# Kernel tuning notes

Hardware: AMD Instinct MI355X
Metric: run time of the kernel (lower is better)

Reference implementation:

```python
import jax, jax.numpy as jnp
import numpy as np

B, T, D_MODEL, H, D = 2, 2048, 2048, 16, 128


def _rope_tables(t, d_half, base=10000.0):
    inv_freq = 1.0 / (base ** (jnp.arange(d_half, dtype=jnp.float32) / d_half))
    ang = jnp.arange(t, dtype=jnp.float32)[:, None] * inv_freq[None, :]  # (T, D/2)
    return jnp.cos(ang), jnp.sin(ang)


def setup_inputs() -> dict:
    key = jax.random.key(0)
    ks = jax.random.split(key, 5)
    x = jax.random.normal(ks[0], (B, T, D_MODEL), dtype=jnp.float32)
    mask = jnp.tril(jnp.ones((T, T), dtype=bool))  # causal boolean mask
    cos, sin = _rope_tables(T, D // 2)
    std = 1.0 / np.sqrt(D_MODEL)
    Wq = jax.random.normal(ks[1], (D_MODEL, H * D), dtype=jnp.float32) * std
    Wk = jax.random.normal(ks[2], (D_MODEL, H * D), dtype=jnp.float32) * std
    Wv = jax.random.normal(ks[3], (D_MODEL, H * D), dtype=jnp.float32) * std
    Wo = jax.random.normal(ks[4], (H * D, D_MODEL), dtype=jnp.float32) * std
    return {"x": x, "mask": mask, "cos": cos, "sin": sin,
            "Wq": Wq, "Wk": Wk, "Wv": Wv, "Wo": Wo}


def _apply_rope(x, cos, sin):
    # x: (B, H, T, D); cos/sin: (T, D/2)
    half = x.shape[-1] // 2
    x1, x2 = x[..., :half], x[..., half:]
    c = cos[None, None]
    s = sin[None, None]
    return jnp.concatenate([x1 * c - x2 * s, x1 * s + x2 * c], axis=-1)


def reference(x, mask, cos, sin, Wq, Wk, Wv, Wo):
    b, t, _ = x.shape
    scale = 1.0 / np.sqrt(D)
    # projections: (B, T, H*D) -> (B, H, T, D)
    q = (x @ Wq).reshape(b, t, H, D).transpose(0, 2, 1, 3)
    k = (x @ Wk).reshape(b, t, H, D).transpose(0, 2, 1, 3)
    v = (x @ Wv).reshape(b, t, H, D).transpose(0, 2, 1, 3)
    q = _apply_rope(q, cos, sin)
    k = _apply_rope(k, cos, sin)
    scores = jnp.einsum('bhqd,bhkd->bhqk', q, k) * scale
    scores = jnp.where(mask[None, None], scores, jnp.float32(-1e30))
    attn = jax.nn.softmax(scores, axis=-1)
    out = jnp.einsum('bhqk,bhkd->bhqd', attn, v)  # (B, H, T, D)
    out = out.transpose(0, 2, 1, 3).reshape(b, t, H * D)
    return out @ Wo
```

## Files before the change

### kernel.cpp

```cpp
#include <hip/hip_runtime.h>

#define T_SEQ 2048
#define DM    2048
#define NH    16
#define HD    128
#define NROW  4096

typedef __attribute__((ext_vector_type(8))) short short8;
typedef __attribute__((ext_vector_type(4))) float f32x4;
typedef __attribute__((ext_vector_type(16))) float f32x16;

static __device__ __forceinline__ float bf2f(unsigned short h) {
    unsigned int u = ((unsigned int)h) << 16;
    return __builtin_bit_cast(float, u);
}
static __device__ __forceinline__ unsigned short f2bf(float f) {
    unsigned int u = __builtin_bit_cast(unsigned int, f);
    u += 0x7FFFu + ((u >> 16) & 1u);
    return (unsigned short)(u >> 16);
}
static __device__ __forceinline__ unsigned short bf_fast(float f) {
    return (unsigned short)((__builtin_bit_cast(unsigned int, f) + 0x8000u) >> 16);
}

typedef __attribute__((address_space(1))) const unsigned int gas_uint;
typedef __attribute__((address_space(3))) unsigned int las_uint;

static __device__ __forceinline__ void load_lds16(const void* g, void* l) {
    __builtin_amdgcn_global_load_lds((gas_uint*)g, (las_uint*)l, 16, 0, 0);
}

static __device__ __forceinline__ f32x4 mfma_bf16(short8 a, short8 b, f32x4 c) {
    return __builtin_amdgcn_mfma_f32_16x16x32_bf16(a, b, c, 0, 0, 0);
}
static __device__ __forceinline__ f32x16 mfma32_bf16(short8 a, short8 b, f32x16 c) {
    return __builtin_amdgcn_mfma_f32_32x32x16_bf16(a, b, c, 0, 0, 0);
}

__global__ __launch_bounds__(256) void k_prep(const float* __restrict__ x,
                                              unsigned short* __restrict__ xb,
                                              const float* __restrict__ w0, const float* __restrict__ w1,
                                              const float* __restrict__ w2, const float* __restrict__ w3,
                                              unsigned short* __restrict__ t0, unsigned short* __restrict__ t1,
                                              unsigned short* __restrict__ t2, unsigned short* __restrict__ t3) {
    const int tid = threadIdx.x;
    const int z = blockIdx.z;
    if (z == 4) {
        const int iblock = blockIdx.y * 32 + blockIdx.x;
#pragma unroll
        for (int i = 0; i < 8; ++i) {
            int idx = (iblock * 2048 + i * 256 + tid) * 4;
            float4 v = *(const float4*)(x + idx);
            ushort4 o;
            o.x = f2bf(v.x); o.y = f2bf(v.y); o.z = f2bf(v.z); o.w = f2bf(v.w);
            *(ushort4*)(xb + idx) = o;
        }
        return;
    }
    __shared__ unsigned short tile[64][68];
    const float* W = (z == 0) ? w0 : (z == 1) ? w1 : (z == 2) ? w2 : w3;
    unsigned short* Wt = (z == 0) ? t0 : (z == 1) ? t1 : (z == 2) ? t2 : t3;
    const int bx = blockIdx.x * 64;
    const int by = blockIdx.y * 64;
    const int rr = tid >> 4, cc = (tid & 15) * 4;
#pragma unroll
    for (int it = 0; it < 4; ++it) {
        int row = it * 16 + rr;
        float4 v = *(const float4*)(W + (size_t)(by + row) * DM + bx + cc);
        ushort4 o;
        o.x = f2bf(v.x); o.y = f2bf(v.y); o.z = f2bf(v.z); o.w = f2bf(v.w);
        *(ushort4*)&tile[row][cc] = o;
    }
    __syncthreads();
#pragma unroll
    for (int it = 0; it < 4; ++it) {
        int ln = it * 16 + rr;
        ushort4 v;
#pragma unroll
        for (int j = 0; j < 4; ++j) v = (j == 0) ? (ushort4){tile[cc][ln], 0, 0, 0} : v, ((unsigned short*)&v)[j] = tile[cc + j][ln];
        *(ushort4*)(Wt + (size_t)(bx + ln) * DM + by + cc) = v;
    }
}

template <bool FOUT>
static __device__ __forceinline__ void gemm_body(const unsigned short* __restrict__ A,
                                                 const unsigned short* __restrict__ Bt,
                                                 unsigned short* __restrict__ Cb,
                                                 float* __restrict__ Cf) {
    __shared__ unsigned short As[128 * 64];
    __shared__ unsigned short Bs[128 * 64];
    const int tid = threadIdx.x;
    const int w = tid >> 6, lane = tid & 63;
    const int col = lane & 15, quad = lane >> 4;
    const int wm = w >> 1, wn = w & 1;
    const size_t m0 = (size_t)blockIdx.y * 128;
    const size_t n0 = (size_t)blockIdx.x * 128;

    f32x4 acc[4][4];
#pragma unroll
    for (int i = 0; i < 4; ++i)
#pragma unroll
        for (int j = 0; j < 4; ++j)
            acc[i][j] = (f32x4){0.f, 0.f, 0.f, 0.f};

    const int lrow = lane >> 3;
    const int gcol = ((lane & 7) ^ lrow) * 8;

    for (int k0 = 0; k0 < DM; k0 += 64) {
#pragma unroll
        for (int c = w; c < 16; c += 4) {
            load_lds16(A + (m0 + c * 8 + lrow) * DM + k0 + gcol, &As[c * 512]);
            load_lds16(Bt + (n0 + c * 8 + lrow) * DM + k0 + gcol, &Bs[c * 512]);
        }
        __syncthreads();
#pragma unroll
        for (int ks = 0; ks < 2; ++ks) {
            short8 af[4], bf[4];
            int g = ks * 4 + quad;
#pragma unroll
            for (int mt = 0; mt < 4; ++mt) {
                int r = wm * 64 + mt * 16 + col;
                af[mt] = *(const short8*)&As[r * 64 + ((g ^ (r & 7)) * 8)];
            }
#pragma unroll
            for (int nt = 0; nt < 4; ++nt) {
                int r = wn * 64 + nt * 16 + col;
                bf[nt] = *(const short8*)&Bs[r * 64 + ((g ^ (r & 7)) * 8)];
            }
#pragma unroll
            for (int mt = 0; mt < 4; ++mt)
#pragma unroll
                for (int nt = 0; nt < 4; ++nt)
                    acc[mt][nt] = mfma_bf16(af[mt], bf[nt], acc[mt][nt]);
        }
        __syncthreads();
    }
#pragma unroll
    for (int mt = 0; mt < 4; ++mt)
#pragma unroll
        for (int nt = 0; nt < 4; ++nt)
#pragma unroll
            for (int reg = 0; reg < 4; ++reg) {
                size_t r = m0 + wm * 64 + mt * 16 + quad * 4 + reg;
                size_t c = n0 + wn * 64 + nt * 16 + col;
                if (FOUT) Cf[r * DM + c] = acc[mt][nt][reg];
                else      Cb[r * DM + c] = f2bf(acc[mt][nt][reg]);
            }
}

__global__ __launch_bounds__(256) void k_gemm_qkv(const unsigned short* __restrict__ xb,
                                                  const unsigned short* __restrict__ wtq,
                                                  const unsigned short* __restrict__ wtk,
                                                  const unsigned short* __restrict__ wtv,
                                                  unsigned short* __restrict__ qb,
                                                  unsigned short* __restrict__ kb,
                                                  unsigned short* __restrict__ vb) {
    int z = blockIdx.z;
    const unsigned short* Bt = (z == 0) ? wtq : (z == 1) ? wtk : wtv;
    unsigned short* C = (z == 0) ? qb : (z == 1) ? kb : vb;
    gemm_body<false>(xb, Bt, C, nullptr);
}

__global__ __launch_bounds__(256) void k_gemm_out(const unsigned short* __restrict__ ob,
                                                  const unsigned short* __restrict__ wto,
                                                  float* __restrict__ out) {
    gemm_body<true>(ob, wto, nullptr, out);
}

__global__ __launch_bounds__(256) void k_rope_k(unsigned short* __restrict__ K,
                                                const float* __restrict__ cosp,
                                                const float* __restrict__ sinp) {
    int idx = blockIdx.x * 256 + threadIdx.x;
    int d4 = (idx & 15) * 4;
    int h = (idx >> 4) & 15;
    int row = idx >> 8;
    int t = row & (T_SEQ - 1);
    size_t base = (size_t)row * DM + h * HD + d4;
    ushort4 x1 = *(const ushort4*)(K + base);
    ushort4 x2 = *(const ushort4*)(K + base + 64);
    float4 c = *(const float4*)(cosp + t * 64 + d4);
    float4 s = *(const float4*)(sinp + t * 64 + d4);
    ushort4 o1, o2;
#pragma unroll
    for (int i = 0; i < 4; ++i) {
        float a1 = bf2f(((const unsigned short*)&x1)[i]);
        float a2 = bf2f(((const unsigned short*)&x2)[i]);
        float cc = ((const float*)&c)[i], ss = ((const float*)&s)[i];
        ((unsigned short*)&o1)[i] = f2bf(a1 * cc - a2 * ss);
        ((unsigned short*)&o2)[i] = f2bf(a1 * ss + a2 * cc);
    }
    *(ushort4*)(K + base) = o1;
    *(ushort4*)(K + base + 64) = o2;
}

__global__ __launch_bounds__(256) void k_vtr(const unsigned short* __restrict__ V,
                                             unsigned short* __restrict__ Vt) {
    __shared__ unsigned short tile[64][68];
    int t0 = blockIdx.x * 64;
    int hd0 = blockIdx.y * 64;
    int b = blockIdx.z;
    int tid = threadIdx.x;
    int rr = tid >> 4, cc = (tid & 15) * 4;
#pragma unroll
    for (int it = 0; it < 4; ++it) {
        int row = it * 16 + rr;
        *(ushort4*)&tile[row][cc] =
            *(const ushort4*)(V + (size_t)(b * T_SEQ + t0 + row) * DM + hd0 + cc);
    }
    __syncthreads();
    int h = hd0 >> 7, d0 = hd0 & 127;
    size_t obase = (size_t)(b * NH + h) * HD;
#pragma unroll
    for (int it = 0; it < 4; ++it) {
        int lhd = it * 16 + rr;
        ushort4 v;
#pragma unroll
        for (int j = 0; j < 4; ++j) ((unsigned short*)&v)[j] = tile[cc + j][lhd];
        *(ushort4*)(Vt + (obase + d0 + lhd) * (size_t)T_SEQ + t0 + cc) = v;
    }
}

#define PST 72
__global__ __launch_bounds__(256) void k_flash(const unsigned short* __restrict__ Q,
                                               const unsigned short* __restrict__ K,
                                               const unsigned short* __restrict__ Vt,
                                               unsigned short* __restrict__ O,
                                               const float* __restrict__ cosp,
                                               const float* __restrict__ sinp) {
    __shared__ unsigned short Ks[64 * 128];
    __shared__ unsigned short Vs[128 * 64];
    __shared__ unsigned short Ps[4][32 * PST];
    const int tid = threadIdx.x;
    const int w = tid >> 6, lane = tid & 63;
    const int col = lane & 31, l5 = lane >> 5;
    const int flat = blockIdx.x | (blockIdx.y << 4) | (blockIdx.z << 8);
    const int j = 15 - (flat >> 5);
    const int hb = flat & 31;
    const int h = hb & 15, b = hb >> 4;
    const int q0 = j * 128;
    const size_t rowbase = ((size_t)b * T_SEQ) * DM + (size_t)h * HD;
    const size_t hbase = ((size_t)b * NH + h) * HD;
    const float SCL = 0.088388347648318447f * 1.4426950408889634f;
    unsigned short* Pw = &Ps[w][0];

    const int t = q0 + w * 32 + col;
    short8 qf[8];
    {
        const unsigned short* qp = Q + rowbase + (size_t)t * DM + l5 * 8;
#pragma unroll
        for (int st = 0; st < 8; ++st)
            qf[st] = *(const short8*)(qp + st * 16);
        const float* cp = cosp + t * 64 + l5 * 8;
        const float* sp = sinp + t * 64 + l5 * 8;
#pragma unroll
        for (int st = 0; st < 4; ++st) {
            float4 c0 = *(const float4*)(cp + st * 16);
            float4 c1 = *(const float4*)(cp + st * 16 + 4);
            float4 s0v = *(const float4*)(sp + st * 16);
            float4 s1v = *(const float4*)(sp + st * 16 + 4);
#pragma unroll
            for (int jj = 0; jj < 8; ++jj) {
                float cv = ((jj < 4) ? ((const float*)&c0)[jj] : ((const float*)&c1)[jj - 4]) * SCL;
                float sv = ((jj < 4) ? ((const float*)&s0v)[jj] : ((const float*)&s1v)[jj - 4]) * SCL;
                float a1 = bf2f((unsigned short)qf[st][jj]);
                float a2 = bf2f((unsigned short)qf[st + 4][jj]);
                qf[st][jj]     = (short)f2bf(a1 * cv - a2 * sv);
                qf[st + 4][jj] = (short)f2bf(a1 * sv + a2 * cv);
            }
        }
    }

    f32x16 o[4];
#pragma unroll
    for (int i = 0; i < 4; ++i) o[i] = (f32x16)(0.f);
    float m_i = -1e30f, l_i = 0.f;

    const int kt_max = 2 * j + 1;
    const int kt_lim = (q0 + w * 32 + 31) >> 6;
    const int cswz = col & 7;

    for (int kt = 0; kt <= kt_max; ++kt) {
        const int k0 = kt * 64;
        __syncthreads();
#pragma unroll
        for (int c = 0; c < 4; ++c) {
            const int c4 = w * 4 + c;
            const int krow = c4 * 4 + (lane >> 4);
            const int kpos = lane & 15;
            load_lds16(K + rowbase + (size_t)(k0 + krow) * DM + ((kpos ^ (krow & 7)) * 8),
                       &Ks[c4 * 512]);
            const int vrow = c4 * 8 + (lane >> 3);
            const int vpos = lane & 7;
            load_lds16(Vt + (hbase + vrow) * (size_t)T_SEQ + k0 + ((vpos ^ (vrow & 7)) * 8),
                       &Vs[c4 * 512]);
        }
        __syncthreads();
        if (kt > kt_lim) continue;

        f32x16 s0 = (f32x16)(0.f), s1 = (f32x16)(0.f);
        __builtin_amdgcn_s_setprio(1);
#pragma unroll
        for (int st = 0; st < 8; ++st) {
            const int dg = (2 * st + l5) ^ cswz;
            short8 kf0 = *(const short8*)&Ks[col * 128 + dg * 8];
            short8 kf1 = *(const short8*)&Ks[col * 128 + 4096 + dg * 8];
            s0 = mfma32_bf16(kf0, qf[st], s0);
            s1 = mfma32_bf16(kf1, qf[st], s1);
        }
        __builtin_amdgcn_s_setprio(0);

        if (k0 + 63 > q0 + w * 32) {
            const int kb = k0 + 4 * l5;
#pragma unroll
            for (int r = 0; r < 16; ++r) {
                const int key = kb + (r & 3) + 8 * (r >> 2);
                if (key > t) s0[r] = -1e30f;
                if (key + 32 > t) s1[r] = -1e30f;
            }
        }

        float mx = -1e30f;
#pragma unroll
        for (int r = 0; r < 16; ++r) mx = fmaxf(mx, fmaxf(s0[r], s1[r]));
        mx = fmaxf(mx, __shfl_xor(mx, 32));
        if (!__all(mx - m_i <= 8.0f)) {
            const float mnew = fmaxf(m_i, mx);
            const float alpha = __builtin_amdgcn_exp2f(m_i - mnew);
            m_i = mnew;
            l_i *= alpha;
#pragma unroll
            for (int i = 0; i < 4; ++i) o[i] *= alpha;
        }
        float sum = 0.f;
#pragma unroll
        for (int r = 0; r < 16; ++r) {
            float p0 = __builtin_amdgcn_exp2f(s0[r] - m_i);
            float p1 = __builtin_amdgcn_exp2f(s1[r] - m_i);
            s0[r] = p0; s1[r] = p1;
            sum += p0 + p1;
        }
        sum += __shfl_xor(sum, 32);
        l_i += sum;

#pragma unroll
        for (int g = 0; g < 4; ++g) {
            ushort4 a4, b4;
#pragma unroll
            for (int i = 0; i < 4; ++i) {
                ((unsigned short*)&a4)[i] = bf_fast(s0[g * 4 + i]);
                ((unsigned short*)&b4)[i] = bf_fast(s1[g * 4 + i]);
            }
            *(ushort4*)(Pw + col * PST + g * 8 + 4 * l5)      = a4;
            *(ushort4*)(Pw + col * PST + 32 + g * 8 + 4 * l5) = b4;
        }
        short8 pb[4];
#pragma unroll
        for (int st = 0; st < 4; ++st)
            pb[st] = *(const short8*)(Pw + col * PST + st * 16 + l5 * 8);

        __builtin_amdgcn_s_setprio(1);
#pragma unroll
        for (int ms = 0; ms < 4; ++ms) {
            const int drow = (ms * 32 + col) * 64;
#pragma unroll
            for (int st = 0; st < 4; ++st) {
                const int kg = (2 * st + l5) ^ cswz;
                short8 vf = *(const short8*)&Vs[drow + kg * 8];
                o[ms] = mfma32_bf16(vf, pb[st], o[ms]);
            }
        }
        __builtin_amdgcn_s_setprio(0);
    }

    const float inv = __builtin_amdgcn_rcpf(l_i);
    unsigned short* op = O + rowbase + (size_t)t * DM;
#pragma unroll
    for (int ms = 0; ms < 4; ++ms)
#pragma unroll
        for (int g = 0; g < 4; ++g) {
            ushort4 st4;
#pragma unroll
            for (int i = 0; i < 4; ++i)
                ((unsigned short*)&st4)[i] = bf_fast(o[ms][g * 4 + i] * inv);
            *(ushort4*)(op + ms * 32 + g * 8 + 4 * l5) = st4;
        }
}

extern "C" void kernel_launch(void* const* d_in, const int* in_sizes, int n_in,
                              void* d_out, int out_size, void* d_ws, size_t ws_size,
                              hipStream_t stream) {
    const float* x    = (const float*)d_in[0];
    const float* cosp = (const float*)d_in[2];
    const float* sinp = (const float*)d_in[3];
    const float* Wq   = (const float*)d_in[4];
    const float* Wk   = (const float*)d_in[5];
    const float* Wv   = (const float*)d_in[6];
    const float* Wo   = (const float*)d_in[7];
    float* out = (float*)d_out;

    unsigned short* xb  = (unsigned short*)d_ws;
    unsigned short* wtq = xb  + (size_t)NROW * DM;
    unsigned short* wtk = wtq + (size_t)DM * DM;
    unsigned short* wtv = wtk + (size_t)DM * DM;
    unsigned short* wto = wtv + (size_t)DM * DM;
    unsigned short* qb  = wto + (size_t)DM * DM;
    unsigned short* kb  = qb  + (size_t)NROW * DM;
    unsigned short* vb  = kb  + (size_t)NROW * DM;
    unsigned short* ob  = vb  + (size_t)NROW * DM;
    unsigned short* vt  = xb;

    hipLaunchKernelGGL(k_prep, dim3(32, 32, 5), dim3(256), 0, stream,
                       x, xb, Wq, Wk, Wv, Wo, wtq, wtk, wtv, wto);
    hipLaunchKernelGGL(k_gemm_qkv, dim3(16, 32, 3), dim3(256), 0, stream,
                       xb, wtq, wtk, wtv, qb, kb, vb);
    hipLaunchKernelGGL(k_rope_k, dim3(4096), dim3(256), 0, stream, kb, cosp, sinp);
    hipLaunchKernelGGL(k_vtr, dim3(32, 32, 2), dim3(256), 0, stream, vb, vt);
    hipLaunchKernelGGL(k_flash, dim3(16, 16, 2), dim3(256), 0, stream,
                       qb, kb, vt, ob, cosp, sinp);
    hipLaunchKernelGGL(k_gemm_out, dim3(16, 32, 1), dim3(256), 0, stream, ob, wto, out);
}
```

Measured before the change: 396.5 us.

## Fuse K RoPE and V transpose into QKV GEMM epilogues

The QKV projection GEMM now has per-slice epilogues. The K slice stages its tile in shared memory and applies RoPE before writing. The V slice writes directly in the transposed (b,h,d,t) layout the flash kernel expects. This removes the separate k_rope_k and k_vtr launches and their extra global read/write passes over K and V. In exchange, the QKV kernel uses more shared memory (about 33 KB), which may reduce occupancy, and the transposed V stores are 4-element strided writes that are less coalesced.

```diff
diff --git a/kernel.cpp b/kernel.cpp
--- a/kernel.cpp
+++ b/kernel.cpp
@@ -82,13 +82,16 @@
     }
 }
 
-template <bool FOUT>
-static __device__ __forceinline__ void gemm_body(const unsigned short* __restrict__ A,
+template <int MODE>
+static __device__ __forceinline__ void gemm_body(unsigned short* smem,
+                                                 const unsigned short* __restrict__ A,
                                                  const unsigned short* __restrict__ Bt,
                                                  unsigned short* __restrict__ Cb,
-                                                 float* __restrict__ Cf) {
-    __shared__ unsigned short As[128 * 64];
-    __shared__ unsigned short Bs[128 * 64];
+                                                 float* __restrict__ Cf,
+                                                 const float* __restrict__ cosp,
+                                                 const float* __restrict__ sinp) {
+    unsigned short* As = smem;
+    unsigned short* Bs = smem + 8192;
     const int tid = threadIdx.x;
     const int w = tid >> 6, lane = tid & 63;
     const int col = lane & 15, quad = lane >> 4;
@@ -135,17 +138,70 @@
         }
         __syncthreads();
     }
-#pragma unroll
-    for (int mt = 0; mt < 4; ++mt)
-#pragma unroll
-        for (int nt = 0; nt < 4; ++nt)
-#pragma unroll
-            for (int reg = 0; reg < 4; ++reg) {
-                size_t r = m0 + wm * 64 + mt * 16 + quad * 4 + reg;
-                size_t c = n0 + wn * 64 + nt * 16 + col;
-                if (FOUT) Cf[r * DM + c] = acc[mt][nt][reg];
-                else      Cb[r * DM + c] = f2bf(acc[mt][nt][reg]);
-            }
+
+    if (MODE == 0 || MODE == 1) {
+#pragma unroll
+        for (int mt = 0; mt < 4; ++mt)
+#pragma unroll
+            for (int nt = 0; nt < 4; ++nt)
+#pragma unroll
+                for (int reg = 0; reg < 4; ++reg) {
+                    size_t r = m0 + wm * 64 + mt * 16 + quad * 4 + reg;
+                    size_t c = n0 + wn * 64 + nt * 16 + col;
+                    if (MODE == 1) Cf[r * DM + c] = acc[mt][nt][reg];
+                    else           Cb[r * DM + c] = f2bf(acc[mt][nt][reg]);
+                }
+    } else if (MODE == 2) {
+        const int bb = (int)(m0 >> 11);
+        const int tb = ((int)m0 & 2047) + wm * 64 + quad * 4;
+#pragma unroll
+        for (int mt = 0; mt < 4; ++mt)
+#pragma unroll
+            for (int nt = 0; nt < 4; ++nt) {
+                const int c = (int)n0 + wn * 64 + nt * 16 + col;
+                ushort4 v;
+#pragma unroll
+                for (int reg = 0; reg < 4; ++reg)
+                    ((unsigned short*)&v)[reg] = f2bf(acc[mt][nt][reg]);
+                *(ushort4*)(Cb + (size_t)(bb * 2048 + c) * T_SEQ + tb + mt * 16) = v;
+            }
+    } else {
+        unsigned short* tile = smem;
+#pragma unroll
+        for (int mt = 0; mt < 4; ++mt)
+#pragma unroll
+            for (int nt = 0; nt < 4; ++nt)
+#pragma unroll
+                for (int reg = 0; reg < 4; ++reg) {
+                    const int rl = wm * 64 + mt * 16 + quad * 4 + reg;
+                    const int cl = wn * 64 + nt * 16 + col;
+                    tile[rl * 132 + cl] = f2bf(acc[mt][nt][reg]);
+                }
+        __syncthreads();
+#pragma unroll
+        for (int i = 0; i < 8; ++i) {
+            const int task = i * 256 + tid;
+            const int rl = task >> 4;
+            const int d4 = (task & 15) * 4;
+            const int r = (int)m0 + rl;
+            const int t = r & (T_SEQ - 1);
+            ushort4 x1 = *(const ushort4*)&tile[rl * 132 + d4];
+            ushort4 x2 = *(const ushort4*)&tile[rl * 132 + d4 + 64];
+            float4 c = *(const float4*)(cosp + t * 64 + d4);
+            float4 s = *(const float4*)(sinp + t * 64 + d4);
+            ushort4 o1, o2;
+#pragma unroll
+            for (int q = 0; q < 4; ++q) {
+                float a1 = bf2f(((const unsigned short*)&x1)[q]);
+                float a2 = bf2f(((const unsigned short*)&x2)[q]);
+                float cc = ((const float*)&c)[q], ss = ((const float*)&s)[q];
+                ((unsigned short*)&o1)[q] = f2bf(a1 * cc - a2 * ss);
+                ((unsigned short*)&o2)[q] = f2bf(a1 * ss + a2 * cc);
+            }
+            *(ushort4*)(Cb + (size_t)r * DM + n0 + d4)      = o1;
+            *(ushort4*)(Cb + (size_t)r * DM + n0 + d4 + 64) = o2;
+        }
+    }
 }
 
 __global__ __launch_bounds__(256) void k_gemm_qkv(const unsigned short* __restrict__ xb,
@@ -154,70 +210,21 @@
                                                   const unsigned short* __restrict__ wtv,
                                                   unsigned short* __restrict__ qb,
                                                   unsigned short* __restrict__ kb,
-                                                  unsigned short* __restrict__ vb) {
-    int z = blockIdx.z;
-    const unsigned short* Bt = (z == 0) ? wtq : (z == 1) ? wtk : wtv;
-    unsigned short* C = (z == 0) ? qb : (z == 1) ? kb : vb;
-    gemm_body<false>(xb, Bt, C, nullptr);
+                                                  unsigned short* __restrict__ vt,
+                                                  const float* __restrict__ cosp,
+                                                  const float* __restrict__ sinp) {
+    __shared__ unsigned short smem[16896];
+    const int z = blockIdx.z;
+    if (z == 0)      gemm_body<0>(smem, xb, wtq, qb, nullptr, nullptr, nullptr);
+    else if (z == 1) gemm_body<3>(smem, xb, wtk, kb, nullptr, cosp, sinp);
+    else             gemm_body<2>(smem, xb, wtv, vt, nullptr, nullptr, nullptr);
 }
 
 __global__ __launch_bounds__(256) void k_gemm_out(const unsigned short* __restrict__ ob,
                                                   const unsigned short* __restrict__ wto,
                                                   float* __restrict__ out) {
-    gemm_body<true>(ob, wto, nullptr, out);
-}
-
-__global__ __launch_bounds__(256) void k_rope_k(unsigned short* __restrict__ K,
-                                                const float* __restrict__ cosp,
-                                                const float* __restrict__ sinp) {
-    int idx = blockIdx.x * 256 + threadIdx.x;
-    int d4 = (idx & 15) * 4;
-    int h = (idx >> 4) & 15;
-    int row = idx >> 8;
-    int t = row & (T_SEQ - 1);
-    size_t base = (size_t)row * DM + h * HD + d4;
-    ushort4 x1 = *(const ushort4*)(K + base);
-    ushort4 x2 = *(const ushort4*)(K + base + 64);
-    float4 c = *(const float4*)(cosp + t * 64 + d4);
-    float4 s = *(const float4*)(sinp + t * 64 + d4);
-    ushort4 o1, o2;
-#pragma unroll
-    for (int i = 0; i < 4; ++i) {
-        float a1 = bf2f(((const unsigned short*)&x1)[i]);
-        float a2 = bf2f(((const unsigned short*)&x2)[i]);
-        float cc = ((const float*)&c)[i], ss = ((const float*)&s)[i];
-        ((unsigned short*)&o1)[i] = f2bf(a1 * cc - a2 * ss);
-        ((unsigned short*)&o2)[i] = f2bf(a1 * ss + a2 * cc);
-    }
-    *(ushort4*)(K + base) = o1;
-    *(ushort4*)(K + base + 64) = o2;
-}
-
-__global__ __launch_bounds__(256) void k_vtr(const unsigned short* __restrict__ V,
-                                             unsigned short* __restrict__ Vt) {
-    __shared__ unsigned short tile[64][68];
-    int t0 = blockIdx.x * 64;
-    int hd0 = blockIdx.y * 64;
-    int b = blockIdx.z;
-    int tid = threadIdx.x;
-    int rr = tid >> 4, cc = (tid & 15) * 4;
-#pragma unroll
-    for (int it = 0; it < 4; ++it) {
-        int row = it * 16 + rr;
-        *(ushort4*)&tile[row][cc] =
-            *(const ushort4*)(V + (size_t)(b * T_SEQ + t0 + row) * DM + hd0 + cc);
-    }
-    __syncthreads();
-    int h = hd0 >> 7, d0 = hd0 & 127;
-    size_t obase = (size_t)(b * NH + h) * HD;
-#pragma unroll
-    for (int it = 0; it < 4; ++it) {
-        int lhd = it * 16 + rr;
-        ushort4 v;
-#pragma unroll
-        for (int j = 0; j < 4; ++j) ((unsigned short*)&v)[j] = tile[cc + j][lhd];
-        *(ushort4*)(Vt + (obase + d0 + lhd) * (size_t)T_SEQ + t0 + cc) = v;
-    }
+    __shared__ unsigned short smem[16384];
+    gemm_body<1>(smem, ob, wto, nullptr, out, nullptr, nullptr);
 }
 
 #define PST 72
@@ -405,16 +412,13 @@
     unsigned short* wto = wtv + (size_t)DM * DM;
     unsigned short* qb  = wto + (size_t)DM * DM;
     unsigned short* kb  = qb  + (size_t)NROW * DM;
-    unsigned short* vb  = kb  + (size_t)NROW * DM;
-    unsigned short* ob  = vb  + (size_t)NROW * DM;
-    unsigned short* vt  = xb;
+    unsigned short* vt  = kb  + (size_t)NROW * DM;
+    unsigned short* ob  = vt  + (size_t)NROW * DM;
 
     hipLaunchKernelGGL(k_prep, dim3(32, 32, 5), dim3(256), 0, stream,
                        x, xb, Wq, Wk, Wv, Wo, wtq, wtk, wtv, wto);
     hipLaunchKernelGGL(k_gemm_qkv, dim3(16, 32, 3), dim3(256), 0, stream,
-                       xb, wtq, wtk, wtv, qb, kb, vb);
-    hipLaunchKernelGGL(k_rope_k, dim3(4096), dim3(256), 0, stream, kb, cosp, sinp);
-    hipLaunchKernelGGL(k_vtr, dim3(32, 32, 2), dim3(256), 0, stream, vb, vt);
+                       xb, wtq, wtk, wtv, qb, kb, vt, cosp, sinp);
     hipLaunchKernelGGL(k_flash, dim3(16, 16, 2), dim3(256), 0, stream,
                        qb, kb, vt, ob, cosp, sinp);
     hipLaunchKernelGGL(k_gemm_out, dim3(16, 32, 1), dim3(256), 0, stream, ob, wto, out);
```

Measured after the change: 382.0 us. 1.04x faster.
